# Kernel tuning notes

Measured on AMD Instinct MI355X. Metric: run time of the kernel, lower is better.

## Reference

```python
import jax, jax.numpy as jnp
import numpy as np

N, E, F_IN, F_OUT = 50000, 1600000, 256, 64
ALPHA = 0.2  # LeakyReLU negative slope


def setup_inputs() -> dict:
    key = jax.random.key(0)
    k1, k2, k3, k4 = jax.random.split(key, 4)
    x = jax.random.normal(k1, (N, F_IN), dtype=jnp.float32)
    edge = jax.random.randint(k2, (2, E), 0, N)  # COO (row, col) indices of adj
    # xavier_normal with gain=1.414 (as in the torch module)
    W = jax.random.normal(k3, (F_IN, F_OUT), dtype=jnp.float32) * (1.414 * np.sqrt(2.0 / (F_IN + F_OUT)))
    a = jax.random.normal(k4, (1, 2 * F_OUT), dtype=jnp.float32) * (1.414 * np.sqrt(2.0 / (1 + 2 * F_OUT)))
    return {"x": x, "edge": edge, "W": W, "a": a}


def reference(x, edge, W, a):
    # eval mode: dropout is a no-op
    Wh = x @ W  # [N, F_OUT]
    src, dst = edge[0], edge[1]
    # a @ concat(Wh[src], Wh[dst]) per edge, computed as two node-level dots then gathered
    s_src = Wh @ a[0, :F_OUT]   # [N]
    s_dst = Wh @ a[0, F_OUT:]   # [N]
    score = s_src[src] + s_dst[dst]                      # [E]
    edge_e = jnp.exp(-jax.nn.leaky_relu(score, ALPHA))   # [E]
    # sparse-softmax denominator: row sums of exp scores
    e_rowsum = jax.ops.segment_sum(edge_e, src, num_segments=N)  # [N]
    # weighted aggregation: h_prime[i] = sum_{(i,j) in E} e_ij * Wh[j]
    h_prime = jax.ops.segment_sum(edge_e[:, None] * Wh[dst], src, num_segments=N)  # [N, F_OUT]
    h_prime = h_prime / e_rowsum[:, None]
    return jax.nn.elu(h_prime)  # concat=True -> ELU
```

## Files before the change

kernel.cpp:

```cpp
#include <hip/hip_runtime.h>
#include <hip/hip_fp16.h>

#define N_NODES 50000
#define N_EDGES 1600000
#define F_IN 256
#define F_OUT 64
#define ALPHA 0.2f

#define BS 64
#define NBK 782
#define NSUB 8
#define CAP 384
#define EB 4096
#define NBB 391
#define LDS_CAP 2560
#define OF_CAP 16384

typedef __attribute__((ext_vector_type(8))) short bf16x8;
typedef __attribute__((ext_vector_type(4))) float f32x4;

__device__ inline unsigned short f2bf(float f) {
    unsigned int u = __float_as_uint(f);
    return (unsigned short)((u + 0x7FFFu + ((u >> 16) & 1u)) >> 16);
}
__device__ inline float bf2f(unsigned short b) {
    return __uint_as_float(((unsigned int)b) << 16);
}

__global__ __launch_bounds__(256) void gat_wprep(
    const float* __restrict__ W, unsigned short* __restrict__ Wf)
{
    const int di = blockIdx.x * 256 + threadIdx.x;
    const int j    = di & 7;
    const int lane = (di >> 3) & 63;
    const int tile = di >> 9;
    const int ks   = tile >> 2;
    const int nt   = tile & 3;
    const int k = ks * 32 + (lane >> 4) * 8 + j;
    const int n = nt * 16 + (lane & 15);
    Wf[di] = f2bf(W[k * F_OUT + n]);
}

__global__ __launch_bounds__(256) void gat_gemm(
    const float* __restrict__ x, const unsigned short* __restrict__ Wf,
    const float* __restrict__ a, unsigned short* __restrict__ Whh,
    float* __restrict__ s_src, float* __restrict__ s_dst)
{
    __shared__ unsigned short Wl[F_IN * F_OUT];
    const int t = threadIdx.x;
    {
        const float4* __restrict__ src = (const float4*)Wf;
        float4* dst = (float4*)Wl;
        #pragma unroll
        for (int i = 0; i < 8; ++i) dst[t + i * 256] = src[t + i * 256];
    }
    __syncthreads();

    const int lane = t & 63;
    const int w    = t >> 6;
    const int q    = lane >> 4;
    const int c16  = lane & 15;
    const bf16x8* __restrict__ Wfrag = (const bf16x8*)Wl;

    float av[4], av2[4];
    #pragma unroll
    for (int nt = 0; nt < 4; ++nt) {
        av[nt]  = a[nt * 16 + c16];
        av2[nt] = a[F_OUT + nt * 16 + c16];
    }

    for (int c = blockIdx.x; c < NBK; c += gridDim.x) {
        const int node0 = c * 64 + w * 16;
        int row = node0 + c16;
        if (row >= N_NODES) row = N_NODES - 1;
        const float4* __restrict__ xp = (const float4*)(x + (size_t)row * F_IN);

        float4 xv[16];
        #pragma unroll
        for (int ks = 0; ks < 8; ++ks) {
            xv[2 * ks]     = xp[ks * 8 + q * 2];
            xv[2 * ks + 1] = xp[ks * 8 + q * 2 + 1];
        }

        f32x4 acc[4];
        #pragma unroll
        for (int nt = 0; nt < 4; ++nt) acc[nt] = (f32x4){0.f, 0.f, 0.f, 0.f};

        #pragma unroll
        for (int ks = 0; ks < 8; ++ks) {
            float xf[8] = {xv[2*ks].x,   xv[2*ks].y,   xv[2*ks].z,   xv[2*ks].w,
                           xv[2*ks+1].x, xv[2*ks+1].y, xv[2*ks+1].z, xv[2*ks+1].w};
            bf16x8 ah, al;
            #pragma unroll
            for (int j = 0; j < 8; ++j) {
                const unsigned short h = f2bf(xf[j]);
                ah[j] = (short)h;
                al[j] = (short)f2bf(xf[j] - bf2f(h));
            }
            #pragma unroll
            for (int nt = 0; nt < 4; ++nt) {
                const bf16x8 bh = Wfrag[(ks * 4 + nt) * 64 + lane];
                acc[nt] = __builtin_amdgcn_mfma_f32_16x16x32_bf16(ah, bh, acc[nt], 0, 0, 0);
                acc[nt] = __builtin_amdgcn_mfma_f32_16x16x32_bf16(al, bh, acc[nt], 0, 0, 0);
            }
        }

        #pragma unroll
        for (int r = 0; r < 4; ++r) {
            const int node = node0 + q * 4 + r;
            float p = 0.f, qq = 0.f;
            #pragma unroll
            for (int nt = 0; nt < 4; ++nt) {
                const float v = acc[nt][r];
                if (node < N_NODES)
                    Whh[(size_t)node * F_OUT + nt * 16 + c16] =
                        __half_as_ushort(__float2half(v));
                p  = fmaf(v, av[nt], p);
                qq = fmaf(v, av2[nt], qq);
            }
            #pragma unroll
            for (int off = 1; off <= 8; off <<= 1) {
                p  += __shfl_xor(p, off);
                qq += __shfl_xor(qq, off);
            }
            if (c16 == 0 && node < N_NODES) { s_src[node] = p; s_dst[node] = qq; }
        }
    }
}

__global__ __launch_bounds__(256) void gat_bucket(
    const int* __restrict__ edge, int* __restrict__ cnt,
    unsigned int* __restrict__ arr, int* __restrict__ of_cnt,
    int2* __restrict__ of_list)
{
    __shared__ int lhist[NBK];
    __shared__ int lstart[NBK + 1];
    __shared__ int gbase[NBK];
    __shared__ int cursor[NBK];
    __shared__ unsigned int sorted[EB];
    __shared__ int scanbuf[256];

    const int t   = threadIdx.x;
    const int blk = blockIdx.x;
    const int e0  = blk * EB;
    const int sub = blk & 7;

    for (int i = t; i < NBK; i += 256) lhist[i] = 0;
    __syncthreads();

    int sreg[EB / 256];
    #pragma unroll
    for (int i = 0; i < EB / 256; ++i) {
        const int e = e0 + i * 256 + t;
        int s = -1;
        if (e < N_EDGES) {
            s = edge[e];
            atomicAdd(&lhist[s >> 6], 1);
        }
        sreg[i] = s;
    }
    __syncthreads();

    int psum = 0;
    {
        const int b0 = t * 4;
        #pragma unroll
        for (int i = 0; i < 4; ++i)
            if (b0 + i < NBK) psum += lhist[b0 + i];
    }
    scanbuf[t] = psum;
    __syncthreads();
    for (int off = 1; off < 256; off <<= 1) {
        const int v = (t >= off) ? scanbuf[t - off] : 0;
        __syncthreads();
        scanbuf[t] += v;
        __syncthreads();
    }
    {
        int run = scanbuf[t] - psum;
        const int b0 = t * 4;
        #pragma unroll
        for (int i = 0; i < 4; ++i) {
            const int b = b0 + i;
            if (b < NBK) {
                lstart[b] = run;
                cursor[b] = run;
                run += lhist[b];
            }
        }
        if (t == 255) lstart[NBK] = scanbuf[255];
    }
    __syncthreads();

    for (int b = t; b < NBK; b += 256) {
        const int c = lhist[b];
        gbase[b] = (c > 0) ? atomicAdd(&cnt[sub * NBK + b], c) : 0;
    }

    #pragma unroll
    for (int i = 0; i < EB / 256; ++i) {
        const int s = sreg[i];
        if (s >= 0) {
            const int e = e0 + i * 256 + t;
            const int d = edge[N_EDGES + e];
            const int b = s >> 6;
            const int pos = atomicAdd(&cursor[b], 1);
            sorted[pos] = ((unsigned)b << 22) | ((unsigned)(s & 63) << 16) | (unsigned)d;
        }
    }
    __syncthreads();

    const int C = lstart[NBK];
    for (int p = t; p < C; p += 256) {
        const unsigned en = sorted[p];
        const int b = (int)(en >> 22);
        const int idx = gbase[b] + (p - lstart[b]);
        if (idx < CAP) {
            arr[((size_t)(sub * NBK + b)) * CAP + idx] = en & 0x3FFFFFu;
        } else {
            const int s = b * 64 + (int)((en >> 16) & 63);
            const int op = atomicAdd(of_cnt, 1);
            if (op < OF_CAP) of_list[op] = make_int2(s, (int)(en & 0xFFFFu));
        }
    }
}

__global__ __launch_bounds__(512) void gat_aggregate(
    const int* __restrict__ cnt, const unsigned int* __restrict__ arr,
    const float* __restrict__ s_src, const float* __restrict__ s_dst,
    const unsigned short* __restrict__ Whh, const int* __restrict__ of_cnt,
    const int2* __restrict__ of_list, float* __restrict__ out)
{
    __shared__ uint2 ent2[LDS_CAP];
    __shared__ int   bin[BS];
    __shared__ int   start[BS + 1];
    __shared__ int   Pl[NSUB + 1];
    const int t = threadIdx.x;
    const int lane = t & 63;
    const int w = t >> 6;
    const int b = blockIdx.x;

    if (t < BS) bin[t] = 0;
    if (w == 0) {
        int c = (lane < NSUB) ? min(cnt[lane * NBK + b], CAP) : 0;
        int s = c;
        #pragma unroll
        for (int off = 1; off < NSUB; off <<= 1) {
            const int v = __shfl_up(s, off);
            if (lane >= off) s += v;
        }
        if (lane < NSUB) Pl[lane + 1] = s;
        if (lane == 0)   Pl[0] = 0;
    }
    __syncthreads();
    const int C = Pl[NSUB];
    const int nof = min(of_cnt[0], OF_CAP);

    unsigned enr[6];
    int nr = 0;
    for (int g = t; g < C; g += 512) {
        int sub = 0;
        #pragma unroll
        for (int s2 = 1; s2 < NSUB; ++s2) sub += (g >= Pl[s2]);
        const unsigned en = arr[((size_t)(sub * NBK + b)) * CAP + (g - Pl[sub])];
        enr[nr++] = en;
        atomicAdd(&bin[en >> 16], 1);
    }
    for (int i = t; i < nof; i += 512) {
        const int2 e2 = of_list[i];
        if ((e2.x >> 6) == b) atomicAdd(&bin[e2.x & 63], 1);
    }
    __syncthreads();
    if (w == 0) {
        const int c = bin[lane];
        int s = c;
        #pragma unroll
        for (int off = 1; off < BS; off <<= 1) {
            const int v = __shfl_up(s, off);
            if (lane >= off) s += v;
        }
        start[lane + 1] = s;
        if (lane == 0) start[0] = 0;
        bin[lane] = s - c;
    }
    __syncthreads();

    for (int r = 0; r < nr; ++r) {
        const unsigned en = enr[r];
        const int sl = (int)(en >> 16);
        const int d  = (int)(en & 0xffffu);
        const float sc = s_src[b * BS + sl] + s_dst[d];
        const float ee = __expf(-(sc > 0.f ? sc : ALPHA * sc));
        const int pos = atomicAdd(&bin[sl], 1);
        if (pos < LDS_CAP) ent2[pos] = make_uint2((unsigned)d, __float_as_uint(ee));
    }
    for (int i = t; i < nof; i += 512) {
        const int2 e2 = of_list[i];
        if ((e2.x >> 6) == b) {
            const float sc = s_src[e2.x] + s_dst[e2.y];
            const float ee = __expf(-(sc > 0.f ? sc : ALPHA * sc));
            const int pos = atomicAdd(&bin[e2.x & 63], 1);
            if (pos < LDS_CAP) ent2[pos] = make_uint2((unsigned)e2.y, __float_as_uint(ee));
        }
    }
    __syncthreads();

    const int q  = lane >> 4;
    const int fq = lane & 15;
    const uint2* __restrict__ Whh2 = (const uint2*)Whh;

    for (int n = w * 8; n < w * 8 + 8; ++n) {
        const int node = b * BS + n;
        if (node >= N_NODES) break;
        const int r0 = start[n];
        const int r1 = min(start[n + 1], LDS_CAP);
        float4 acc = make_float4(0.f, 0.f, 0.f, 0.f);
        float rsum = 0.f;
        for (int j = r0; j < r1; j += 32) {
            float et[8];
            uint2 wv[8];
            #pragma unroll
            for (int k = 0; k < 8; ++k) {
                const int jj = j + 4 * k + q;
                const uint2 e = ent2[min(jj, r1 - 1)];
                et[k] = (jj < r1) ? __uint_as_float(e.y) : 0.f;
                wv[k] = Whh2[(size_t)e.x * 16 + fq];
            }
            #pragma unroll
            for (int k = 0; k < 8; ++k) {
                const __half2* hp = (const __half2*)&wv[k];
                const float2 lo = __half22float2(hp[0]);
                const float2 hi = __half22float2(hp[1]);
                acc.x = fmaf(et[k], lo.x, acc.x);
                acc.y = fmaf(et[k], lo.y, acc.y);
                acc.z = fmaf(et[k], hi.x, acc.z);
                acc.w = fmaf(et[k], hi.y, acc.w);
                rsum += et[k];
            }
        }
        acc.x += __shfl_xor(acc.x, 16); acc.x += __shfl_xor(acc.x, 32);
        acc.y += __shfl_xor(acc.y, 16); acc.y += __shfl_xor(acc.y, 32);
        acc.z += __shfl_xor(acc.z, 16); acc.z += __shfl_xor(acc.z, 32);
        acc.w += __shfl_xor(acc.w, 16); acc.w += __shfl_xor(acc.w, 32);
        rsum  += __shfl_xor(rsum, 16);  rsum  += __shfl_xor(rsum, 32);

        float4 v;
        v.x = acc.x / rsum; v.y = acc.y / rsum;
        v.z = acc.z / rsum; v.w = acc.w / rsum;
        v.x = v.x > 0.f ? v.x : (__expf(v.x) - 1.f);
        v.y = v.y > 0.f ? v.y : (__expf(v.y) - 1.f);
        v.z = v.z > 0.f ? v.z : (__expf(v.z) - 1.f);
        v.w = v.w > 0.f ? v.w : (__expf(v.w) - 1.f);
        if (q == 0)
            ((float4*)out)[(size_t)node * 16 + fq] = v;
    }
}

extern "C" void kernel_launch(void* const* d_in, const int* in_sizes, int n_in,
                              void* d_out, int out_size, void* d_ws, size_t ws_size,
                              hipStream_t stream) {
    const float* x    = (const float*)d_in[0];
    const int*   edge = (const int*)  d_in[1];
    const float* W    = (const float*)d_in[2];
    const float* a    = (const float*)d_in[3];
    float* out = (float*)d_out;

    unsigned short* Whh   = (unsigned short*)d_ws;
    unsigned int*   arr   = (unsigned int*)(Whh + (size_t)N_NODES * F_OUT);
    float*          s_src = (float*)(arr + (size_t)NSUB * NBK * CAP);
    float*          s_dst = s_src + N_NODES;
    int*            cnt   = (int*)(s_dst + N_NODES);
    int2*           of_list = (int2*)(cnt + NSUB * NBK);
    int*            of_cnt  = (int*)(of_list + OF_CAP);
    unsigned short* Wf      = (unsigned short*)(of_cnt + 4);

    hipMemsetAsync(cnt, 0, (size_t)NSUB * NBK * sizeof(int), stream);
    hipMemsetAsync(of_cnt, 0, sizeof(int), stream);

    gat_wprep<<<64, 256, 0, stream>>>(W, Wf);
    gat_gemm<<<782, 256, 0, stream>>>(x, Wf, a, Whh, s_src, s_dst);
    gat_bucket<<<NBB, 256, 0, stream>>>(edge, cnt, arr, of_cnt, of_list);
    gat_aggregate<<<NBK, 512, 0, stream>>>(cnt, arr, s_src, s_dst, Whh,
                                           of_cnt, of_list, out);
}
```

Before: 171.4 us.

## Fuse GEMM and edge bucketing into one launch, fold memsets, pad aggregation lists

The GEMM and edge-bucketing kernels are merged into one grid, with the block index picking which role each block plays, so the two independent stages overlap. The two memsets move into the weight-prep kernel, which removes two launches. In the aggregation kernel, each node's edge list is padded to a multiple of 32 with zero entries, which drops the per-element bounds checks. The fp16 converts plus FMAs are replaced with v_fma_mix inline asm, and the division becomes a multiply by a reciprocal. The trade-offs are a larger LDS footprint (LDS_CAP grows to 4096), which may cut occupancy, and an approximate reciprocal.

```diff
diff --git a/kernel.cpp b/kernel.cpp
--- a/kernel.cpp
+++ b/kernel.cpp
@@ -13,7 +13,7 @@
 #define CAP 384
 #define EB 4096
 #define NBB 391
-#define LDS_CAP 2560
+#define LDS_CAP 4096
 #define OF_CAP 16384
 
 typedef __attribute__((ext_vector_type(8))) short bf16x8;
@@ -27,10 +27,22 @@
     return __uint_as_float(((unsigned int)b) << 16);
 }
 
+__device__ inline void fmix_lo(float& a, unsigned int u, float s) {
+    asm("v_fma_mix_f32 %0, %1, %2, %0 op_sel:[0,0,0] op_sel_hi:[1,0,0]"
+        : "+v"(a) : "v"(u), "v"(s));
+}
+__device__ inline void fmix_hi(float& a, unsigned int u, float s) {
+    asm("v_fma_mix_f32 %0, %1, %2, %0 op_sel:[1,0,0] op_sel_hi:[1,0,0]"
+        : "+v"(a) : "v"(u), "v"(s));
+}
+
 __global__ __launch_bounds__(256) void gat_wprep(
-    const float* __restrict__ W, unsigned short* __restrict__ Wf)
+    const float* __restrict__ W, unsigned short* __restrict__ Wf,
+    int* __restrict__ cnt, int* __restrict__ of_cnt)
 {
     const int di = blockIdx.x * 256 + threadIdx.x;
+    if (di < NSUB * NBK) cnt[di] = 0;
+    if (di == 0) of_cnt[0] = 0;
     const int j    = di & 7;
     const int lane = (di >> 3) & 63;
     const int tile = di >> 9;
@@ -41,35 +53,41 @@
     Wf[di] = f2bf(W[k * F_OUT + n]);
 }
 
-__global__ __launch_bounds__(256) void gat_gemm(
+__global__ __launch_bounds__(256) void gat_fused(
     const float* __restrict__ x, const unsigned short* __restrict__ Wf,
     const float* __restrict__ a, unsigned short* __restrict__ Whh,
-    float* __restrict__ s_src, float* __restrict__ s_dst)
+    float* __restrict__ s_src, float* __restrict__ s_dst,
+    const int* __restrict__ edge, int* __restrict__ cnt,
+    unsigned int* __restrict__ arr, int* __restrict__ of_cnt,
+    int2* __restrict__ of_list)
 {
-    __shared__ unsigned short Wl[F_IN * F_OUT];
+    __shared__ __align__(16) unsigned char smem[32768];
     const int t = threadIdx.x;
-    {
-        const float4* __restrict__ src = (const float4*)Wf;
-        float4* dst = (float4*)Wl;
-        #pragma unroll
-        for (int i = 0; i < 8; ++i) dst[t + i * 256] = src[t + i * 256];
-    }
-    __syncthreads();
-
-    const int lane = t & 63;
-    const int w    = t >> 6;
-    const int q    = lane >> 4;
-    const int c16  = lane & 15;
-    const bf16x8* __restrict__ Wfrag = (const bf16x8*)Wl;
-
-    float av[4], av2[4];
-    #pragma unroll
-    for (int nt = 0; nt < 4; ++nt) {
-        av[nt]  = a[nt * 16 + c16];
-        av2[nt] = a[F_OUT + nt * 16 + c16];
-    }
-
-    for (int c = blockIdx.x; c < NBK; c += gridDim.x) {
+
+    if (blockIdx.x < NBK) {
+        unsigned short* Wl = (unsigned short*)smem;
+        {
+            const float4* __restrict__ src = (const float4*)Wf;
+            float4* dst = (float4*)Wl;
+            #pragma unroll
+            for (int i = 0; i < 8; ++i) dst[t + i * 256] = src[t + i * 256];
+        }
+        __syncthreads();
+
+        const int lane = t & 63;
+        const int w    = t >> 6;
+        const int q    = lane >> 4;
+        const int c16  = lane & 15;
+        const bf16x8* __restrict__ Wfrag = (const bf16x8*)Wl;
+
+        float av[4], av2[4];
+        #pragma unroll
+        for (int nt = 0; nt < 4; ++nt) {
+            av[nt]  = a[nt * 16 + c16];
+            av2[nt] = a[F_OUT + nt * 16 + c16];
+        }
+
+        const int c = blockIdx.x;
         const int node0 = c * 64 + w * 16;
         int row = node0 + c16;
         if (row >= N_NODES) row = N_NODES - 1;
@@ -125,102 +143,95 @@
             }
             if (c16 == 0 && node < N_NODES) { s_src[node] = p; s_dst[node] = qq; }
         }
-    }
-}
-
-__global__ __launch_bounds__(256) void gat_bucket(
-    const int* __restrict__ edge, int* __restrict__ cnt,
-    unsigned int* __restrict__ arr, int* __restrict__ of_cnt,
-    int2* __restrict__ of_list)
-{
-    __shared__ int lhist[NBK];
-    __shared__ int lstart[NBK + 1];
-    __shared__ int gbase[NBK];
-    __shared__ int cursor[NBK];
-    __shared__ unsigned int sorted[EB];
-    __shared__ int scanbuf[256];
-
-    const int t   = threadIdx.x;
-    const int blk = blockIdx.x;
-    const int e0  = blk * EB;
-    const int sub = blk & 7;
-
-    for (int i = t; i < NBK; i += 256) lhist[i] = 0;
-    __syncthreads();
-
-    int sreg[EB / 256];
-    #pragma unroll
-    for (int i = 0; i < EB / 256; ++i) {
-        const int e = e0 + i * 256 + t;
-        int s = -1;
-        if (e < N_EDGES) {
-            s = edge[e];
-            atomicAdd(&lhist[s >> 6], 1);
-        }
-        sreg[i] = s;
-    }
-    __syncthreads();
-
-    int psum = 0;
-    {
-        const int b0 = t * 4;
-        #pragma unroll
-        for (int i = 0; i < 4; ++i)
-            if (b0 + i < NBK) psum += lhist[b0 + i];
-    }
-    scanbuf[t] = psum;
-    __syncthreads();
-    for (int off = 1; off < 256; off <<= 1) {
-        const int v = (t >= off) ? scanbuf[t - off] : 0;
-        __syncthreads();
-        scanbuf[t] += v;
-        __syncthreads();
-    }
-    {
-        int run = scanbuf[t] - psum;
-        const int b0 = t * 4;
-        #pragma unroll
-        for (int i = 0; i < 4; ++i) {
-            const int b = b0 + i;
-            if (b < NBK) {
-                lstart[b] = run;
-                cursor[b] = run;
-                run += lhist[b];
-            }
-        }
-        if (t == 255) lstart[NBK] = scanbuf[255];
-    }
-    __syncthreads();
-
-    for (int b = t; b < NBK; b += 256) {
-        const int c = lhist[b];
-        gbase[b] = (c > 0) ? atomicAdd(&cnt[sub * NBK + b], c) : 0;
-    }
-
-    #pragma unroll
-    for (int i = 0; i < EB / 256; ++i) {
-        const int s = sreg[i];
-        if (s >= 0) {
+    } else {
+        int* lhist            = (int*)smem;
+        int* lstart           = (int*)(smem + 3128);
+        int* gbase            = (int*)(smem + 6260);
+        int* cursor           = (int*)(smem + 9388);
+        int* scanbuf          = (int*)(smem + 12516);
+        unsigned int* sorted  = (unsigned int*)(smem + 13540);
+
+        const int blk = blockIdx.x - NBK;
+        const int e0  = blk * EB;
+        const int sub = blk & 7;
+
+        for (int i = t; i < NBK; i += 256) lhist[i] = 0;
+        __syncthreads();
+
+        int sreg[EB / 256];
+        #pragma unroll
+        for (int i = 0; i < EB / 256; ++i) {
             const int e = e0 + i * 256 + t;
-            const int d = edge[N_EDGES + e];
-            const int b = s >> 6;
-            const int pos = atomicAdd(&cursor[b], 1);
-            sorted[pos] = ((unsigned)b << 22) | ((unsigned)(s & 63) << 16) | (unsigned)d;
-        }
-    }
-    __syncthreads();
-
-    const int C = lstart[NBK];
-    for (int p = t; p < C; p += 256) {
-        const unsigned en = sorted[p];
-        const int b = (int)(en >> 22);
-        const int idx = gbase[b] + (p - lstart[b]);
-        if (idx < CAP) {
-            arr[((size_t)(sub * NBK + b)) * CAP + idx] = en & 0x3FFFFFu;
-        } else {
-            const int s = b * 64 + (int)((en >> 16) & 63);
-            const int op = atomicAdd(of_cnt, 1);
-            if (op < OF_CAP) of_list[op] = make_int2(s, (int)(en & 0xFFFFu));
+            int s = -1;
+            if (e < N_EDGES) {
+                s = edge[e];
+                atomicAdd(&lhist[s >> 6], 1);
+            }
+            sreg[i] = s;
+        }
+        __syncthreads();
+
+        int psum = 0;
+        {
+            const int b0 = t * 4;
+            #pragma unroll
+            for (int i = 0; i < 4; ++i)
+                if (b0 + i < NBK) psum += lhist[b0 + i];
+        }
+        scanbuf[t] = psum;
+        __syncthreads();
+        for (int off = 1; off < 256; off <<= 1) {
+            const int v = (t >= off) ? scanbuf[t - off] : 0;
+            __syncthreads();
+            scanbuf[t] += v;
+            __syncthreads();
+        }
+        {
+            int run = scanbuf[t] - psum;
+            const int b0 = t * 4;
+            #pragma unroll
+            for (int i = 0; i < 4; ++i) {
+                const int b = b0 + i;
+                if (b < NBK) {
+                    lstart[b] = run;
+                    cursor[b] = run;
+                    run += lhist[b];
+                }
+            }
+            if (t == 255) lstart[NBK] = scanbuf[255];
+        }
+        __syncthreads();
+
+        for (int b = t; b < NBK; b += 256) {
+            const int c = lhist[b];
+            gbase[b] = (c > 0) ? atomicAdd(&cnt[sub * NBK + b], c) : 0;
+        }
+
+        #pragma unroll
+        for (int i = 0; i < EB / 256; ++i) {
+            const int s = sreg[i];
+            if (s >= 0) {
+                const int e = e0 + i * 256 + t;
+                const int d = edge[N_EDGES + e];
+                const int b = s >> 6;
+                const int pos = atomicAdd(&cursor[b], 1);
+                sorted[pos] = ((unsigned)b << 22) | ((unsigned)(s & 63) << 16) | (unsigned)d;
+            }
+        }
+        __syncthreads();
+
+        const int C = lstart[NBK];
+        for (int p = t; p < C; p += 256) {
+            const unsigned en = sorted[p];
+            const int b = (int)(en >> 22);
+            const int idx = gbase[b] + (p - lstart[b]);
+            if (idx < CAP) {
+                arr[((size_t)(sub * NBK + b)) * CAP + idx] = en & 0x3FFFFFu;
+            } else {
+                const int s = b * 64 + (int)((en >> 16) & 63);
+                const int op = atomicAdd(of_cnt, 1);
+                if (op < OF_CAP) of_list[op] = make_int2(s, (int)(en & 0xFFFFu));
+            }
         }
     }
 }
@@ -231,7 +242,7 @@
     const unsigned short* __restrict__ Whh, const int* __restrict__ of_cnt,
     const int2* __restrict__ of_list, float* __restrict__ out)
 {
-    __shared__ uint2 ent2[LDS_CAP];
+    __shared__ uint2 ent2[LDS_CAP + 32];
     __shared__ int   bin[BS];
     __shared__ int   start[BS + 1];
     __shared__ int   Pl[NSUB + 1];
@@ -241,6 +252,7 @@
     const int b = blockIdx.x;
 
     if (t < BS) bin[t] = 0;
+    if (t < 32) ent2[LDS_CAP + t] = make_uint2(0u, 0u);
     if (w == 0) {
         int c = (lane < NSUB) ? min(cnt[lane * NBK + b], CAP) : 0;
         int s = c;
@@ -272,8 +284,9 @@
     }
     __syncthreads();
     if (w == 0) {
-        const int c = bin[lane];
-        int s = c;
+        const int c  = bin[lane];
+        const int pc = (c + 31) & ~31;
+        int s = pc;
         #pragma unroll
         for (int off = 1; off < BS; off <<= 1) {
             const int v = __shfl_up(s, off);
@@ -281,7 +294,7 @@
         }
         start[lane + 1] = s;
         if (lane == 0) start[0] = 0;
-        bin[lane] = s - c;
+        bin[lane] = s - pc;
     }
     __syncthreads();
 
@@ -304,6 +317,13 @@
         }
     }
     __syncthreads();
+    {
+        const int n  = t & 63;
+        const int e1 = min(start[n + 1], LDS_CAP);
+        for (int p = bin[n] + (t >> 6); p < e1; p += 8)
+            ent2[p] = make_uint2(0u, 0u);
+    }
+    __syncthreads();
 
     const int q  = lane >> 4;
     const int fq = lane & 15;
@@ -317,25 +337,22 @@
         float4 acc = make_float4(0.f, 0.f, 0.f, 0.f);
         float rsum = 0.f;
         for (int j = r0; j < r1; j += 32) {
-            float et[8];
+            unsigned eu[8];
             uint2 wv[8];
             #pragma unroll
             for (int k = 0; k < 8; ++k) {
-                const int jj = j + 4 * k + q;
-                const uint2 e = ent2[min(jj, r1 - 1)];
-                et[k] = (jj < r1) ? __uint_as_float(e.y) : 0.f;
+                const uint2 e = ent2[j + 4 * k + q];
+                eu[k] = e.y;
                 wv[k] = Whh2[(size_t)e.x * 16 + fq];
             }
             #pragma unroll
             for (int k = 0; k < 8; ++k) {
-                const __half2* hp = (const __half2*)&wv[k];
-                const float2 lo = __half22float2(hp[0]);
-                const float2 hi = __half22float2(hp[1]);
-                acc.x = fmaf(et[k], lo.x, acc.x);
-                acc.y = fmaf(et[k], lo.y, acc.y);
-                acc.z = fmaf(et[k], hi.x, acc.z);
-                acc.w = fmaf(et[k], hi.y, acc.w);
-                rsum += et[k];
+                const float et = __uint_as_float(eu[k]);
+                fmix_lo(acc.x, wv[k].x, et);
+                fmix_hi(acc.y, wv[k].x, et);
+                fmix_lo(acc.z, wv[k].y, et);
+                fmix_hi(acc.w, wv[k].y, et);
+                rsum += et;
             }
         }
         acc.x += __shfl_xor(acc.x, 16); acc.x += __shfl_xor(acc.x, 32);
@@ -344,9 +361,10 @@
         acc.w += __shfl_xor(acc.w, 16); acc.w += __shfl_xor(acc.w, 32);
         rsum  += __shfl_xor(rsum, 16);  rsum  += __shfl_xor(rsum, 32);
 
+        const float rinv = __builtin_amdgcn_rcpf(rsum);
         float4 v;
-        v.x = acc.x / rsum; v.y = acc.y / rsum;
-        v.z = acc.z / rsum; v.w = acc.w / rsum;
+        v.x = acc.x * rinv; v.y = acc.y * rinv;
+        v.z = acc.z * rinv; v.w = acc.w * rinv;
         v.x = v.x > 0.f ? v.x : (__expf(v.x) - 1.f);
         v.y = v.y > 0.f ? v.y : (__expf(v.y) - 1.f);
         v.z = v.z > 0.f ? v.z : (__expf(v.z) - 1.f);
@@ -374,12 +392,9 @@
     int*            of_cnt  = (int*)(of_list + OF_CAP);
     unsigned short* Wf      = (unsigned short*)(of_cnt + 4);
 
-    hipMemsetAsync(cnt, 0, (size_t)NSUB * NBK * sizeof(int), stream);
-    hipMemsetAsync(of_cnt, 0, sizeof(int), stream);
-
-    gat_wprep<<<64, 256, 0, stream>>>(W, Wf);
-    gat_gemm<<<782, 256, 0, stream>>>(x, Wf, a, Whh, s_src, s_dst);
-    gat_bucket<<<NBB, 256, 0, stream>>>(edge, cnt, arr, of_cnt, of_list);
+    gat_wprep<<<64, 256, 0, stream>>>(W, Wf, cnt, of_cnt);
+    gat_fused<<<NBK + NBB, 256, 0, stream>>>(x, Wf, a, Whh, s_src, s_dst,
+                                             edge, cnt, arr, of_cnt, of_list);
     gat_aggregate<<<NBK, 512, 0, stream>>>(cnt, arr, s_src, s_dst, Whh,
                                            of_cnt, of_list, out);
 }
```

Result: faster. 154.7 us (-9.7%).
